# Performance work log

Measured on AMD Instinct MI355X. Metric: run time of the kernel, lower is better.

The kernel has to match this reference:

```python
import jax, jax.numpy as jnp
import numpy as np

B, C, H, W = 2, 64, 64, 64
C2 = C // 2
N = H * W


def conv1x1(x, w, b):
    # x: (B,Cin,H,W), w: (Cout,Cin), b: (Cout,)
    return jnp.einsum('bchw,oc->bohw', x, w) + b[None, :, None, None]


def setup_inputs() -> dict:
    key = jax.random.key(0)
    ks = jax.random.split(key, 20)
    s = 0.05
    d = {
        'x1': jax.random.normal(ks[0], (B, C, H, W), jnp.float32),
        'x2': jax.random.normal(ks[1], (B, C, H, W), jnp.float32),
        'wq1': jax.random.normal(ks[2], (C2, C), jnp.float32) * s,
        'bq1': jax.random.normal(ks[3], (C2,), jnp.float32) * s,
        'wk1': jax.random.normal(ks[4], (C2, C), jnp.float32) * s,
        'bk1': jax.random.normal(ks[5], (C2,), jnp.float32) * s,
        'wv1': jax.random.normal(ks[6], (C2, C), jnp.float32) * s,
        'bv1': jax.random.normal(ks[7], (C2,), jnp.float32) * s,
        'wc1': jax.random.normal(ks[8], (C, C2), jnp.float32) * s,
        'bc1': jax.random.normal(ks[9], (C,), jnp.float32) * s,
        'wq2': jax.random.normal(ks[10], (C2, C), jnp.float32) * s,
        'bq2': jax.random.normal(ks[11], (C2,), jnp.float32) * s,
        'wk2': jax.random.normal(ks[12], (C2, C), jnp.float32) * s,
        'bk2': jax.random.normal(ks[13], (C2,), jnp.float32) * s,
        'wv2': jax.random.normal(ks[14], (C2, C), jnp.float32) * s,
        'bv2': jax.random.normal(ks[15], (C2,), jnp.float32) * s,
        'wc2': jax.random.normal(ks[16], (C, C2), jnp.float32) * s,
        'bc2': jax.random.normal(ks[17], (C,), jnp.float32) * s,
        'gamma1': jax.random.normal(ks[18], (1,), jnp.float32) * 0.5,
        'gamma2': jax.random.normal(ks[19], (1,), jnp.float32) * 0.5,
    }
    return d


def reference(x1, x2, wq1, bq1, wk1, bk1, wv1, bv1, wc1, bc1,
              wq2, bq2, wk2, bk2, wv2, bv2, wc2, bc2, gamma1, gamma2):
    b, c, h, w = x1.shape
    n = h * w
    # branch-1 projections (boundary semantics)
    q1 = jnp.max(conv1x1(x1, wq1, bq1), axis=1).reshape(b, n)          # (B,N) channel-max
    k1 = jnp.max(conv1x1(x1, wk1, bk1).reshape(b, -1, n), axis=1)      # (B,N)
    v1 = conv1x1(x1, wv1, bv1).reshape(b, -1, n)                        # (B,C/2,N)
    # branch-2 projections (field semantics)
    q2 = jnp.mean(conv1x1(x2, wq2, bq2), axis=1).reshape(b, n)         # (B,N) channel-mean
    k2 = jnp.mean(conv1x1(x2, wk2, bk2).reshape(b, -1, n), axis=1)     # (B,N)
    v2 = conv1x1(x2, wv2, bv2).reshape(b, -1, n)                        # (B,C/2,N)
    # energy2 = q1 (B,N,1) @ k2 (B,1,N) outer product; inverted sigmoid gate
    att2 = 1.0 - jax.nn.sigmoid(q1[:, :, None] * k2[:, None, :])        # (B,N,N)
    out1 = jnp.einsum('bck,bmk->bcm', v1, att2).reshape(b, c // 2, h, w)
    out1 = conv1x1(out1, wc2, bc2)
    # energy1 = q2 outer k1; sigmoid gate
    att1 = jax.nn.sigmoid(q2[:, :, None] * k1[:, None, :])              # (B,N,N)
    out2 = jnp.einsum('bck,bmk->bcm', v2, att1).reshape(b, c // 2, h, w)
    out2 = conv1x1(out2, wc1, bc1)
    out1 = x1 + gamma1[0] * out1
    out2 = x2 + gamma2[0] * out2
    return (out1, out2)
```

## Files before the change

kernel.cpp:

```cpp
#include <hip/hip_runtime.h>
#include <hip/hip_bf16.h>

#define NN 4096
#define CC 64
#define C2 32
#define BB 2

#define M_BLK  32
#define KBLK   64
#define KB_ITERS (NN / KBLK)

#define WS_Q1 0
#define WS_K1 8192
#define WS_Q2 16384
#define WS_K2 24576
#define WS_V1 32768
#define WS_V2 163840

typedef __attribute__((address_space(1))) const unsigned int GUI;
typedef __attribute__((address_space(3))) unsigned int LUI;
typedef __attribute__((ext_vector_type(8))) short bf16x8;
typedef __attribute__((ext_vector_type(4))) float f32x4;

__device__ __forceinline__ void glds16(const void* g, void* l) {
    __builtin_amdgcn_global_load_lds((GUI*)g, (LUI*)l, 16, 0, 0);
}

__device__ __forceinline__ unsigned short bf16_rne(float f) {
    union { float f; unsigned u; } x; x.f = f;
    unsigned u = x.u + 0x7fff + ((x.u >> 16) & 1);
    return (unsigned short)(u >> 16);
}
__device__ __forceinline__ unsigned pack2(float a, float b) {
    __hip_bfloat162 h = __float22bfloat162_rn(make_float2(a, b));
    unsigned r; __builtin_memcpy(&r, &h, 4); return r;
}
__device__ __forceinline__ float sigm_e2(float x) {
    return __builtin_amdgcn_rcpf(1.0f + __builtin_amdgcn_exp2f(x));
}

__global__ __launch_bounds__(256) void proj_kernel(
    const float* __restrict__ x1, const float* __restrict__ x2,
    const float* __restrict__ wq1, const float* __restrict__ bq1,
    const float* __restrict__ wk1, const float* __restrict__ bk1,
    const float* __restrict__ wv1, const float* __restrict__ bv1,
    const float* __restrict__ wq2, const float* __restrict__ bq2,
    const float* __restrict__ wk2, const float* __restrict__ bk2,
    const float* __restrict__ wv2, const float* __restrict__ bv2,
    float* __restrict__ ws)
{
    const int ln = threadIdx.x & 63;
    const int og = threadIdx.x >> 6;
    const int n  = blockIdx.x * 64 + ln;
    const int p  = blockIdx.y;
    const int b  = blockIdx.z;

    const float* x; const float* w; const float* bias;
    int mode; float* dstf; unsigned short* dstv;
    switch (p) {
      case 0: x = x1; w = wq1; bias = bq1; mode = 0; dstf = ws + WS_Q1; dstv = 0; break;
      case 1: x = x1; w = wk1; bias = bk1; mode = 0; dstf = ws + WS_K1; dstv = 0; break;
      case 2: x = x1; w = wv1; bias = bv1; mode = 2; dstf = 0; dstv = (unsigned short*)(ws + WS_V1); break;
      case 3: x = x2; w = wq2; bias = bq2; mode = 1; dstf = ws + WS_Q2; dstv = 0; break;
      case 4: x = x2; w = wk2; bias = bk2; mode = 1; dstf = ws + WS_K2; dstv = 0; break;
      default:x = x2; w = wv2; bias = bv2; mode = 2; dstf = 0; dstv = (unsigned short*)(ws + WS_V2); break;
    }

    __shared__ float red[4][C2][64];

    float acc[C2];
    #pragma unroll
    for (int o = 0; o < C2; ++o) acc[o] = 0.0f;

    const float* xb = x + ((size_t)b * CC + og * 16) * NN + n;
    #pragma unroll
    for (int ci = 0; ci < 16; ++ci) {
        const float xv = xb[(size_t)ci * NN];
        #pragma unroll
        for (int o = 0; o < C2; ++o)
            acc[o] += w[o * CC + og * 16 + ci] * xv;
    }
    #pragma unroll
    for (int o = 0; o < C2; ++o) red[og][o][ln] = acc[o];
    __syncthreads();

    float f[8];
    #pragma unroll
    for (int j = 0; j < 8; ++j) {
        const int o = og * 8 + j;
        f[j] = red[0][o][ln] + red[1][o][ln] + red[2][o][ln] + red[3][o][ln]
             + bias[o];
    }

    if (mode == 2) {
        #pragma unroll
        for (int j = 0; j < 8; ++j)
            dstv[((size_t)b * C2 + og * 8 + j) * NN + n] = bf16_rne(f[j]);
    } else {
        float r;
        if (mode == 0) {
            r = f[0];
            #pragma unroll
            for (int j = 1; j < 8; ++j) r = fmaxf(r, f[j]);
        } else {
            r = 0.0f;
            #pragma unroll
            for (int j = 0; j < 8; ++j) r += f[j];
        }
        __syncthreads();
        red[og][0][ln] = r;
        __syncthreads();
        if (og == 0) {
            const float a0 = red[0][0][ln], a1 = red[1][0][ln];
            const float a2 = red[2][0][ln], a3 = red[3][0][ln];
            const float rr = (mode == 0)
                ? fmaxf(fmaxf(a0, a1), fmaxf(a2, a3))
                : (a0 + a1 + a2 + a3) * (1.0f / C2);
            dstf[(size_t)b * NN + n] = rr;
        }
    }
}

__global__ __launch_bounds__(256) void attn_mfma(
    const float* __restrict__ q1, const float* __restrict__ k1,
    const float* __restrict__ q2, const float* __restrict__ k2,
    const unsigned short* __restrict__ v1, const unsigned short* __restrict__ v2,
    const float* __restrict__ x1,  const float* __restrict__ x2,
    const float* __restrict__ wc1, const float* __restrict__ bc1,
    const float* __restrict__ wc2, const float* __restrict__ bc2,
    const float* __restrict__ g1,  const float* __restrict__ g2,
    float* __restrict__ out)
{
    __shared__ unsigned short vtile[2][C2 * KBLK];
    __shared__ unsigned short stile[2][M_BLK * KBLK];

    const int tid = threadIdx.x;
    const int wv  = tid >> 6;
    const int ln  = tid & 63;

    const int z      = blockIdx.y;
    const int branch = z & 1;
    const int b      = z >> 1;
    const int m0     = blockIdx.x * M_BLK;

    const float* q; const float* kv; const unsigned short* vbf; float sl2e;
    if (branch == 0) { q = q1; kv = k2; vbf = v1; sl2e =  1.44269504089f; }
    else             { q = q2; kv = k1; vbf = v2; sl2e = -1.44269504089f; }

    const int sm = tid & 31;
    const int sc = tid >> 5;
    const float qs = q[(size_t)b * NN + m0 + sm] * sl2e;
    const float* kvb = kv + (size_t)b * NN;

    f32x4 acc[2];
    #pragma unroll
    for (int mt = 0; mt < 2; ++mt) acc[mt] = (f32x4){0.f, 0.f, 0.f, 0.f};

    const int vc = tid >> 3;
    const int vs = tid & 7;
    const unsigned short* vsrc0 = vbf + (size_t)(b * C2 + vc) * NN
                                + ((vs ^ (vc & 7)) << 3);

    auto sigPackWrite = [&](int buf, float4 ka, float4 kb4) {
        float s[8];
        s[0] = sigm_e2(qs * ka.x);  s[1] = sigm_e2(qs * ka.y);
        s[2] = sigm_e2(qs * ka.z);  s[3] = sigm_e2(qs * ka.w);
        s[4] = sigm_e2(qs * kb4.x); s[5] = sigm_e2(qs * kb4.y);
        s[6] = sigm_e2(qs * kb4.z); s[7] = sigm_e2(qs * kb4.w);

        uint4 w;
        w.x = pack2(s[0], s[1]); w.y = pack2(s[2], s[3]);
        w.z = pack2(s[4], s[5]); w.w = pack2(s[6], s[7]);

        char* srow = (char*)stile[buf] + sm * 128;
        *(uint4*)(srow + ((sc ^ (sm & 7)) << 4)) = w;
    };

    glds16(vsrc0, (char*)vtile[0] + tid * 16);
    {
        const float* kvp = kvb + sc * 8;
        sigPackWrite(0, *(const float4*)(kvp), *(const float4*)(kvp + 4));
    }
    asm volatile("s_waitcnt vmcnt(0)" ::: "memory");
    __syncthreads();

    const int ct  = wv & 1;
    const int ks  = wv >> 1;
    const int col = (ks << 2) + (ln >> 4);
    const int ac  = ct * 16 + (ln & 15);

    for (int kb = 0; kb < KB_ITERS; ++kb) {
        const int cur = kb & 1;
        const bool more = (kb + 1 < KB_ITERS);

        float4 ka, kb4;
        if (more) {
            glds16(vsrc0 + (kb + 1) * KBLK,
                   (char*)vtile[cur ^ 1] + tid * 16);
            const float* kvp = kvb + (kb + 1) * KBLK + sc * 8;
            ka  = *(const float4*)(kvp);
            kb4 = *(const float4*)(kvp + 4);
        }

        const bf16x8 af = *(const bf16x8*)((const char*)vtile[cur]
                          + ac * 128 + ((col ^ (ac & 7)) << 4));
        #pragma unroll
        for (int mt = 0; mt < 2; ++mt) {
            const int bm = mt * 16 + (ln & 15);
            const bf16x8 bfr = *(const bf16x8*)((const char*)stile[cur]
                               + bm * 128 + ((col ^ (bm & 7)) << 4));
            acc[mt] = __builtin_amdgcn_mfma_f32_16x16x32_bf16(af, bfr, acc[mt], 0, 0, 0);
        }

        if (more) sigPackWrite(cur ^ 1, ka, kb4);

        asm volatile("s_waitcnt vmcnt(0)" ::: "memory");
        __syncthreads();
    }

    float* red = (float*)stile;
    if (wv >= 2) {
        #pragma unroll
        for (int mt = 0; mt < 2; ++mt)
            *(f32x4*)&red[((wv - 2) * 2 + mt) * 256 + ln * 4] = acc[mt];
    }
    __syncthreads();
    float* s_lds = (float*)vtile;
    if (wv < 2) {
        #pragma unroll
        for (int mt = 0; mt < 2; ++mt) {
            const f32x4 o = *(const f32x4*)&red[(wv * 2 + mt) * 256 + ln * 4];
            acc[mt].x += o.x; acc[mt].y += o.y; acc[mt].z += o.z; acc[mt].w += o.w;
            #pragma unroll
            for (int j = 0; j < 4; ++j) {
                const int c = wv * 16 + (ln >> 4) * 4 + j;
                const int m = mt * 16 + (ln & 15);
                s_lds[c * M_BLK + m] = acc[mt][j];
            }
        }
    }
    __syncthreads();

    const float* wmat; const float* bias; const float* x; float gamma;
    float* o;
    if (branch == 0) { wmat = wc2; bias = bc2; x = x1; gamma = g1[0]; o = out; }
    else             { wmat = wc1; bias = bc1; x = x2; gamma = g2[0];
                       o = out + (size_t)BB * CC * NN; }

    const int m  = tid & 31;
    const int cg = tid >> 5;

    float sv[C2];
    #pragma unroll
    for (int c = 0; c < C2; ++c) sv[c] = s_lds[c * M_BLK + m];

    #pragma unroll
    for (int j = 0; j < 8; ++j) {
        const int co = cg * 8 + j;
        float a = bias[co];
        #pragma unroll
        for (int c = 0; c < C2; ++c)
            a += wmat[co * C2 + c] * sv[c];
        const size_t idx = ((size_t)b * CC + co) * NN + m0 + m;
        o[idx] = x[idx] + gamma * a;
    }
}

extern "C" void kernel_launch(void* const* d_in, const int* in_sizes, int n_in,
                              void* d_out, int out_size, void* d_ws, size_t ws_size,
                              hipStream_t stream)
{
    const float* x1  = (const float*)d_in[0];
    const float* x2  = (const float*)d_in[1];
    const float* wq1 = (const float*)d_in[2];
    const float* bq1 = (const float*)d_in[3];
    const float* wk1 = (const float*)d_in[4];
    const float* bk1 = (const float*)d_in[5];
    const float* wv1 = (const float*)d_in[6];
    const float* bv1 = (const float*)d_in[7];
    const float* wc1 = (const float*)d_in[8];
    const float* bc1 = (const float*)d_in[9];
    const float* wq2 = (const float*)d_in[10];
    const float* bq2 = (const float*)d_in[11];
    const float* wk2 = (const float*)d_in[12];
    const float* bk2 = (const float*)d_in[13];
    const float* wv2 = (const float*)d_in[14];
    const float* bv2 = (const float*)d_in[15];
    const float* wc2 = (const float*)d_in[16];
    const float* bc2 = (const float*)d_in[17];
    const float* g1  = (const float*)d_in[18];
    const float* g2  = (const float*)d_in[19];

    float* ws  = (float*)d_ws;
    float* out = (float*)d_out;

    proj_kernel<<<dim3(NN / 64, 6, BB), 256, 0, stream>>>(
        x1, x2, wq1, bq1, wk1, bk1, wv1, bv1,
        wq2, bq2, wk2, bk2, wv2, bv2, ws);

    const float* q1 = ws + WS_Q1; const float* k1 = ws + WS_K1;
    const float* q2 = ws + WS_Q2; const float* k2 = ws + WS_K2;
    const unsigned short* v1 = (const unsigned short*)(ws + WS_V1);
    const unsigned short* v2 = (const unsigned short*)(ws + WS_V2);

    attn_mfma<<<dim3(NN / M_BLK, BB * 2), 256, 0, stream>>>(
        q1, k1, q2, k2, v1, v2,
        x1, x2, wc1, bc1, wc2, bc2, g1, g2, out);
}
```

Measured before the change: 61.35 us.

## Halve attention row block to 16 rows to double workgroup count

Reduces M_BLK from 32 to 16, so each workgroup computes one 16-row MFMA tile instead of two, and the grid doubles. The sigmoid tile generation, LDS swizzled store (now 8-byte writes), reduction and output conv epilogue are rewritten for the smaller tile. The aim is more workgroups to fill the GPU's CUs. In exchange, each V tile loaded into LDS is reused half as much, so V traffic per output doubles.

```diff
diff --git a/kernel.cpp b/kernel.cpp
--- a/kernel.cpp
+++ b/kernel.cpp
@@ -6,7 +6,7 @@
 #define C2 32
 #define BB 2
 
-#define M_BLK  32
+#define M_BLK  16
 #define KBLK   64
 #define KB_ITERS (NN / KBLK)
 
@@ -147,40 +147,32 @@
     if (branch == 0) { q = q1; kv = k2; vbf = v1; sl2e =  1.44269504089f; }
     else             { q = q2; kv = k1; vbf = v2; sl2e = -1.44269504089f; }
 
-    const int sm = tid & 31;
-    const int sc = tid >> 5;
+    const int sm = tid & 15;
+    const int sc = tid >> 4;
     const float qs = q[(size_t)b * NN + m0 + sm] * sl2e;
     const float* kvb = kv + (size_t)b * NN;
 
-    f32x4 acc[2];
-    #pragma unroll
-    for (int mt = 0; mt < 2; ++mt) acc[mt] = (f32x4){0.f, 0.f, 0.f, 0.f};
+    f32x4 acc = (f32x4){0.f, 0.f, 0.f, 0.f};
 
     const int vc = tid >> 3;
     const int vs = tid & 7;
     const unsigned short* vsrc0 = vbf + (size_t)(b * C2 + vc) * NN
                                 + ((vs ^ (vc & 7)) << 3);
 
-    auto sigPackWrite = [&](int buf, float4 ka, float4 kb4) {
-        float s[8];
+    auto sigPackWrite = [&](int buf, float4 ka) {
+        float s[4];
         s[0] = sigm_e2(qs * ka.x);  s[1] = sigm_e2(qs * ka.y);
         s[2] = sigm_e2(qs * ka.z);  s[3] = sigm_e2(qs * ka.w);
-        s[4] = sigm_e2(qs * kb4.x); s[5] = sigm_e2(qs * kb4.y);
-        s[6] = sigm_e2(qs * kb4.z); s[7] = sigm_e2(qs * kb4.w);
-
-        uint4 w;
+
+        uint2 w;
         w.x = pack2(s[0], s[1]); w.y = pack2(s[2], s[3]);
-        w.z = pack2(s[4], s[5]); w.w = pack2(s[6], s[7]);
 
         char* srow = (char*)stile[buf] + sm * 128;
-        *(uint4*)(srow + ((sc ^ (sm & 7)) << 4)) = w;
+        *(uint2*)(srow + ((((sc >> 1) ^ (sm & 7)) << 4) + ((sc & 1) << 3))) = w;
     };
 
     glds16(vsrc0, (char*)vtile[0] + tid * 16);
-    {
-        const float* kvp = kvb + sc * 8;
-        sigPackWrite(0, *(const float4*)(kvp), *(const float4*)(kvp + 4));
-    }
+    sigPackWrite(0, *(const float4*)(kvb + sc * 4));
     asm volatile("s_waitcnt vmcnt(0)" ::: "memory");
     __syncthreads();
 
@@ -188,55 +180,43 @@
     const int ks  = wv >> 1;
     const int col = (ks << 2) + (ln >> 4);
     const int ac  = ct * 16 + (ln & 15);
+    const int bm  = ln & 15;
 
     for (int kb = 0; kb < KB_ITERS; ++kb) {
         const int cur = kb & 1;
         const bool more = (kb + 1 < KB_ITERS);
 
-        float4 ka, kb4;
+        float4 ka;
         if (more) {
             glds16(vsrc0 + (kb + 1) * KBLK,
                    (char*)vtile[cur ^ 1] + tid * 16);
-            const float* kvp = kvb + (kb + 1) * KBLK + sc * 8;
-            ka  = *(const float4*)(kvp);
-            kb4 = *(const float4*)(kvp + 4);
+            ka = *(const float4*)(kvb + (kb + 1) * KBLK + sc * 4);
         }
 
         const bf16x8 af = *(const bf16x8*)((const char*)vtile[cur]
                           + ac * 128 + ((col ^ (ac & 7)) << 4));
-        #pragma unroll
-        for (int mt = 0; mt < 2; ++mt) {
-            const int bm = mt * 16 + (ln & 15);
-            const bf16x8 bfr = *(const bf16x8*)((const char*)stile[cur]
-                               + bm * 128 + ((col ^ (bm & 7)) << 4));
-            acc[mt] = __builtin_amdgcn_mfma_f32_16x16x32_bf16(af, bfr, acc[mt], 0, 0, 0);
-        }
-
-        if (more) sigPackWrite(cur ^ 1, ka, kb4);
+        const bf16x8 bfr = *(const bf16x8*)((const char*)stile[cur]
+                           + bm * 128 + ((col ^ (bm & 7)) << 4));
+        acc = __builtin_amdgcn_mfma_f32_16x16x32_bf16(af, bfr, acc, 0, 0, 0);
+
+        if (more) sigPackWrite(cur ^ 1, ka);
 
         asm volatile("s_waitcnt vmcnt(0)" ::: "memory");
         __syncthreads();
     }
 
     float* red = (float*)stile;
-    if (wv >= 2) {
-        #pragma unroll
-        for (int mt = 0; mt < 2; ++mt)
-            *(f32x4*)&red[((wv - 2) * 2 + mt) * 256 + ln * 4] = acc[mt];
-    }
+    if (wv >= 2)
+        *(f32x4*)&red[(wv - 2) * 256 + ln * 4] = acc;
     __syncthreads();
     float* s_lds = (float*)vtile;
     if (wv < 2) {
-        #pragma unroll
-        for (int mt = 0; mt < 2; ++mt) {
-            const f32x4 o = *(const f32x4*)&red[(wv * 2 + mt) * 256 + ln * 4];
-            acc[mt].x += o.x; acc[mt].y += o.y; acc[mt].z += o.z; acc[mt].w += o.w;
-            #pragma unroll
-            for (int j = 0; j < 4; ++j) {
-                const int c = wv * 16 + (ln >> 4) * 4 + j;
-                const int m = mt * 16 + (ln & 15);
-                s_lds[c * M_BLK + m] = acc[mt][j];
-            }
+        const f32x4 o = *(const f32x4*)&red[wv * 256 + ln * 4];
+        acc.x += o.x; acc.y += o.y; acc.z += o.z; acc.w += o.w;
+        #pragma unroll
+        for (int j = 0; j < 4; ++j) {
+            const int c = wv * 16 + (ln >> 4) * 4 + j;
+            s_lds[c * M_BLK + (ln & 15)] = acc[j];
         }
     }
     __syncthreads();
@@ -247,16 +227,16 @@
     else             { wmat = wc1; bias = bc1; x = x2; gamma = g2[0];
                        o = out + (size_t)BB * CC * NN; }
 
-    const int m  = tid & 31;
-    const int cg = tid >> 5;
+    const int m  = tid & 15;
+    const int ch = tid >> 4;
 
     float sv[C2];
     #pragma unroll
     for (int c = 0; c < C2; ++c) sv[c] = s_lds[c * M_BLK + m];
 
     #pragma unroll
-    for (int j = 0; j < 8; ++j) {
-        const int co = cg * 8 + j;
+    for (int j = 0; j < 4; ++j) {
+        const int co = ch * 4 + j;
         float a = bias[co];
         #pragma unroll
         for (int c = 0; c < C2; ++c)
```

Result: faster. 57.90 us (-5.6%).
